# Kernel tuning notes

Measured on AMD Instinct MI355X. Metric: run time of the kernel, lower is better.

Reference implementation:

```python
import jax, jax.numpy as jnp
import numpy as np

THRESHOLD = 0.1
N_HEAD = 16
NEG_INF = -1e9


def setup_inputs() -> dict:
    key = jax.random.key(0)
    ks = jax.random.split(key, 8)
    B, T, C = 2, 2048, 1024
    H, D, R = N_HEAD, C // N_HEAD, 8
    return {
        "x": jax.random.normal(ks[0], (B, T, C), dtype=jnp.float32),
        "W_attn": jax.random.normal(ks[1], (C, 3 * C), dtype=jnp.float32) * 0.02,
        "W_proj": jax.random.normal(ks[2], (C, C), dtype=jnp.float32) * 0.02,
        "W_recip": jax.random.normal(ks[3], (D, R), dtype=jnp.float32) * 0.02,
        "w_std": jax.random.uniform(ks[4], (H,), dtype=jnp.float32),
        "w_rec": jax.random.uniform(ks[5], (H,), dtype=jnp.float32),
        "w_disc": jax.random.uniform(ks[6], (H,), dtype=jnp.float32),
        "d_bias": jax.random.normal(ks[7], (H, T), dtype=jnp.float32) * 0.02,
    }


def reference(x, W_attn, W_proj, W_recip, w_std, w_rec, w_disc, d_bias):
    B, T, C = x.shape
    H = N_HEAD
    D = C // H
    R = W_recip.shape[1]
    D_std = D - R

    # QKV projection (Linear without bias)
    qkv = x @ W_attn  # [B,T,3C]
    q, k, v = jnp.split(qkv, 3, axis=2)

    def to_heads(t):
        return t.reshape(B, T, H, D).transpose(0, 2, 1, 3)  # [B,H,T,D]

    q, k, v = to_heads(q), to_heads(k), to_heads(v)

    # low-rank reciprocal projections
    QW = q @ W_recip  # [B,H,T,R]
    KW = k @ W_recip

    ws = jnp.sqrt(jnp.clip(w_std, 1e-8))[:, None, None]  # [H,1,1]
    wr = jnp.sqrt(jnp.clip(w_rec, 1e-8))[:, None, None]
    use_ra = (w_rec > THRESHOLD)[:, None, None]  # [H,1,1]

    # RA heads: augmented Q/K = [ws*Q_std | wr*KW] / [ws*K_std | wr*QW]
    q_aug = jnp.concatenate([ws * q[..., :D_std], wr * KW], axis=-1)
    k_aug = jnp.concatenate([ws * k[..., :D_std], wr * QW], axis=-1)
    q_eff = jnp.where(use_ra, q_aug, ws * q)
    k_eff = jnp.where(use_ra, k_aug, ws * k)

    # mean-centered discoverability column bias: [1,H,1,T]
    d = d_bias[:, :T]
    d = d - d.mean(axis=-1, keepdims=True)
    bias = (d * w_disc[:, None])[None, :, None, :]

    scale = 1.0 / jnp.sqrt(jnp.asarray(D, dtype=x.dtype))
    scores = jnp.einsum("bhid,bhjd->bhij", q_eff, k_eff) * scale + bias
    causal = jnp.tril(jnp.ones((T, T), dtype=bool))
    scores = jnp.where(causal[None, None], scores, NEG_INF)
    attn = jax.nn.softmax(scores, axis=-1)
    out = jnp.einsum("bhij,bhjd->bhid", attn, v)  # [B,H,T,D]

    out = out.transpose(0, 2, 1, 3).reshape(B, T, C)
    return out @ W_proj
```

## Files before the change

### kernel.cpp

```cpp
#include <hip/hip_runtime.h>
#include <hip/hip_bf16.h>

#define DEVI __device__ __forceinline__

typedef __attribute__((ext_vector_type(8))) short short8;
typedef __attribute__((ext_vector_type(4))) short short4v;
typedef __attribute__((ext_vector_type(4))) float floatx4;

static constexpr int B_ = 2, T_ = 2048, C_ = 1024, H_ = 16, D_ = 64;
static constexpr float LOG2E = 1.44269504088896f;

DEVI float bf2f(unsigned short u) {
    union { unsigned int i; float f; } v; v.i = ((unsigned int)u) << 16; return v.f;
}
DEVI unsigned short f2bf(float f) {
    union { float f; unsigned int i; } v; v.f = f;
    unsigned int x = v.i;
    return (unsigned short)((x + 0x7fffu + ((x >> 16) & 1u)) >> 16);
}
DEVI unsigned int pk2bf(float lo, float hi) {
#if __has_builtin(__builtin_amdgcn_cvt_pk_bf16_f32)
    typedef __attribute__((ext_vector_type(2))) __bf16 bf16x2;
    union { bf16x2 v; unsigned int u; } r;
    r.v = __builtin_amdgcn_cvt_pk_bf16_f32(lo, hi);
    return r.u;
#else
    return (unsigned int)f2bf(lo) | ((unsigned int)f2bf(hi) << 16);
#endif
}
DEVI float fast_exp2(float x) {
#if __has_builtin(__builtin_amdgcn_exp2f)
    return __builtin_amdgcn_exp2f(x);
#else
    return __expf(x * 0.6931471805599453f);
#endif
}

DEVI void async16(const unsigned short* g, unsigned short* l) {
    __builtin_amdgcn_global_load_lds((const __attribute__((address_space(1))) void*)g,
                                     (__attribute__((address_space(3))) void*)l, 16, 0, 0);
}

DEVI void tr_body(const float* in, unsigned short* out, int K, int N, int bx, int by,
                  int tid, float (*tile)[65]) {
    int k0 = by * 64, n0 = bx * 64;
#pragma unroll
    for (int r = 0; r < 4; r++) {
        int ci = tid + r * 256;
        int row = ci >> 4, c4 = (ci & 15) * 4;
        float4 v = *(const float4*)&in[(size_t)(k0 + row) * N + n0 + c4];
        tile[row][c4 + 0] = v.x; tile[row][c4 + 1] = v.y;
        tile[row][c4 + 2] = v.z; tile[row][c4 + 3] = v.w;
    }
    __syncthreads();
#pragma unroll
    for (int r = 0; r < 2; r++) {
        int ci = tid + r * 256;
        int row = ci >> 3, c8 = (ci & 7) * 8;
        union { unsigned short u[8]; short8 s; } o;
#pragma unroll
        for (int j = 0; j < 8; j++) o.u[j] = f2bf(tile[c8 + j][row]);
        *(short8*)&out[(size_t)(n0 + row) * K + k0 + c8] = o.s;
    }
}

__global__ __launch_bounds__(256) void k_prep(const float* __restrict__ x,
                                              const float* __restrict__ W_attn,
                                              const float* __restrict__ W_proj,
                                              const float* __restrict__ d_bias,
                                              const float* __restrict__ w_disc,
                                              unsigned short* __restrict__ x_bf,
                                              unsigned short* __restrict__ wa_t,
                                              unsigned short* __restrict__ wp_t,
                                              float* __restrict__ bias) {
    __shared__ float tile[64][65];
    __shared__ float red[256];
    int bid = blockIdx.x, tid = threadIdx.x;
    if (bid < 2048) {
        int i = bid * 256 + tid;
        const float4* p = (const float4*)x + (size_t)i * 2;
        float4 a = p[0], b = p[1];
        union { unsigned short u[8]; short8 s; } r;
        r.u[0] = f2bf(a.x); r.u[1] = f2bf(a.y); r.u[2] = f2bf(a.z); r.u[3] = f2bf(a.w);
        r.u[4] = f2bf(b.x); r.u[5] = f2bf(b.y); r.u[6] = f2bf(b.z); r.u[7] = f2bf(b.w);
        *(short8*)&x_bf[(size_t)i * 8] = r.s;
    } else if (bid < 2816) {
        int idx = bid - 2048;
        tr_body(W_attn, wa_t, 1024, 3072, idx % 48, idx / 48, tid, tile);
    } else if (bid < 3072) {
        int idx = bid - 2816;
        tr_body(W_proj, wp_t, 1024, 1024, idx & 15, idx >> 4, tid, tile);
    } else {
        int h = bid - 3072;
        float s = 0.f;
        for (int t = tid; t < T_; t += 256) s += d_bias[h * T_ + t];
        red[tid] = s;
        __syncthreads();
        for (int st = 128; st > 0; st >>= 1) {
            if (tid < st) red[tid] += red[tid + st];
            __syncthreads();
        }
        float mean = red[0] * (1.0f / T_);
        float wd = w_disc[h] * LOG2E;
        for (int t = tid; t < T_; t += 256) bias[h * T_ + t] = (d_bias[h * T_ + t] - mean) * wd;
    }
}

template <typename OUT>
__global__ __launch_bounds__(256) void k_gemm(const unsigned short* __restrict__ A,
                                              const unsigned short* __restrict__ Bt,
                                              OUT* __restrict__ C, int M, int N, int K) {
    __shared__ __align__(16) unsigned short As[128 * 32];
    __shared__ __align__(16) unsigned short Bs[128 * 32];
    int m0 = blockIdx.y * 128, n0 = blockIdx.x * 128;
    int tid = threadIdx.x, l = tid & 63, w = tid >> 6;
    int wm = (w >> 1) * 64, wn = (w & 1) * 64;
    int lm = l & 15, lq = l >> 4;
    floatx4 acc[4][4];
#pragma unroll
    for (int a = 0; a < 4; a++)
#pragma unroll
        for (int b = 0; b < 4; b++) acc[a][b] = {0.f, 0.f, 0.f, 0.f};

    for (int k0 = 0; k0 < K; k0 += 32) {
        __syncthreads();
#pragma unroll
        for (int r = 0; r < 2; r++) {
            int ci = tid + r * 256;
            int row = ci >> 2, off = (ci & 3) * 8;
            async16(&A[(size_t)(m0 + row) * K + k0 + off], &As[row * 32 + off]);
            async16(&Bt[(size_t)(n0 + row) * K + k0 + off], &Bs[row * 32 + off]);
        }
        __syncthreads();
        short8 af[4], bf[4];
#pragma unroll
        for (int t = 0; t < 4; t++) af[t] = *(short8*)&As[(wm + t * 16 + lm) * 32 + lq * 8];
#pragma unroll
        for (int t = 0; t < 4; t++) bf[t] = *(short8*)&Bs[(wn + t * 16 + lm) * 32 + lq * 8];
#pragma unroll
        for (int tm = 0; tm < 4; tm++)
#pragma unroll
            for (int tn = 0; tn < 4; tn++)
                acc[tm][tn] = __builtin_amdgcn_mfma_f32_16x16x32_bf16(af[tm], bf[tn], acc[tm][tn], 0, 0, 0);
    }
#pragma unroll
    for (int tm = 0; tm < 4; tm++)
#pragma unroll
        for (int tn = 0; tn < 4; tn++) {
            int row = m0 + wm + tm * 16 + lq * 4;
            int col = n0 + wn + tn * 16 + lm;
#pragma unroll
            for (int r = 0; r < 4; r++) {
                float v = acc[tm][tn][r];
                if constexpr (sizeof(OUT) == 2) C[(size_t)(row + r) * N + col] = (OUT)f2bf(v);
                else                            C[(size_t)(row + r) * N + col] = v;
            }
        }
}

__global__ __launch_bounds__(256) void k_gemm64(const unsigned short* __restrict__ A,
                                                const unsigned short* __restrict__ Bt,
                                                float* __restrict__ C, int M, int N, int K) {
    __shared__ __align__(16) unsigned short As[128 * 32];
    __shared__ __align__(16) unsigned short Bs[64 * 32];
    int m0 = blockIdx.y * 128, n0 = blockIdx.x * 64;
    int tid = threadIdx.x, l = tid & 63, w = tid >> 6;
    int wm = w * 32;
    int lm = l & 15, lq = l >> 4;
    floatx4 acc[2][4];
#pragma unroll
    for (int a = 0; a < 2; a++)
#pragma unroll
        for (int b = 0; b < 4; b++) acc[a][b] = {0.f, 0.f, 0.f, 0.f};

    for (int k0 = 0; k0 < K; k0 += 32) {
        __syncthreads();
#pragma unroll
        for (int r = 0; r < 2; r++) {
            int ci = tid + r * 256;
            int row = ci >> 2, off = (ci & 3) * 8;
            async16(&A[(size_t)(m0 + row) * K + k0 + off], &As[row * 32 + off]);
        }
        {
            int row = tid >> 2, off = (tid & 3) * 8;
            async16(&Bt[(size_t)(n0 + row) * K + k0 + off], &Bs[row * 32 + off]);
        }
        __syncthreads();
        short8 af[2], bf[4];
#pragma unroll
        for (int t = 0; t < 2; t++) af[t] = *(short8*)&As[(wm + t * 16 + lm) * 32 + lq * 8];
#pragma unroll
        for (int t = 0; t < 4; t++) bf[t] = *(short8*)&Bs[(t * 16 + lm) * 32 + lq * 8];
#pragma unroll
        for (int tm = 0; tm < 2; tm++)
#pragma unroll
            for (int tn = 0; tn < 4; tn++)
                acc[tm][tn] = __builtin_amdgcn_mfma_f32_16x16x32_bf16(af[tm], bf[tn], acc[tm][tn], 0, 0, 0);
    }
#pragma unroll
    for (int tm = 0; tm < 2; tm++)
#pragma unroll
        for (int tn = 0; tn < 4; tn++) {
            int row = m0 + wm + tm * 16 + lq * 4;
            int col = n0 + tn * 16 + lm;
#pragma unroll
            for (int r = 0; r < 4; r++) C[(size_t)(row + r) * N + col] = acc[tm][tn][r];
        }
}

DEVI void build_body(const unsigned short* qkv, const float* Wr, const float* w_std,
                     const float* w_rec, unsigned short* qe, unsigned short* ke, int g) {
    int t = g & (T_ - 1), h = (g >> 11) & (H_ - 1), b = g >> 15;
    float ws = sqrtf(fmaxf(w_std[h], 1e-8f));
    float wr = sqrtf(fmaxf(w_rec[h], 1e-8f));
    bool ra = w_rec[h] > 0.1f;
    const unsigned short* qrow = qkv + (size_t)(b * T_ + t) * 3072 + h * 64;
    const unsigned short* krow = qrow + 1024;
    float q[64], k[64];
#pragma unroll
    for (int i = 0; i < 8; i++) {
        short8 qv = *(const short8*)&qrow[i * 8];
        short8 kv = *(const short8*)&krow[i * 8];
#pragma unroll
        for (int j = 0; j < 8; j++) {
            q[i * 8 + j] = bf2f((unsigned short)qv[j]);
            k[i * 8 + j] = bf2f((unsigned short)kv[j]);
        }
    }
    float QW[8], KW[8];
#pragma unroll
    for (int r = 0; r < 8; r++) { QW[r] = 0.f; KW[r] = 0.f; }
#pragma unroll
    for (int d = 0; d < 64; d++)
#pragma unroll
        for (int r = 0; r < 8; r++) {
            QW[r] += q[d] * Wr[d * 8 + r];
            KW[r] += k[d] * Wr[d * 8 + r];
        }
    const float qscale = 0.125f * LOG2E;
    size_t tbase = (size_t)(b * H_ + h) * 131072 + (size_t)(t >> 4) * 1024 + (size_t)(t & 15) * 8;
#pragma unroll
    for (int i = 0; i < 8; i++) {
        union { unsigned short u[8]; short8 s; } uq, uk;
#pragma unroll
        for (int j = 0; j < 8; j++) {
            int d = i * 8 + j;
            float qv, kv;
            if (ra && d >= 56) { qv = wr * KW[d - 56]; kv = wr * QW[d - 56]; }
            else               { qv = ws * q[d];       kv = ws * k[d]; }
            uq.u[j] = f2bf(qv * qscale);
            uk.u[j] = f2bf(kv);
        }
        size_t off = tbase + (size_t)(i >> 2) * 512 + (size_t)(i & 3) * 128;
        *(short8*)&qe[off] = uq.s;
        *(short8*)&ke[off] = uk.s;
    }
}

__global__ __launch_bounds__(256) void k_bv(const unsigned short* __restrict__ qkv,
                                            const float* __restrict__ W_recip,
                                            const float* __restrict__ w_std,
                                            const float* __restrict__ w_rec,
                                            unsigned short* __restrict__ qe,
                                            unsigned short* __restrict__ ke,
                                            unsigned short* __restrict__ vt) {
    __shared__ float Wr[64 * 8];
    int bid = blockIdx.x, tid = threadIdx.x;
    if (bid < 256) {
        for (int i = tid; i < 512; i += 256) Wr[i] = W_recip[i];
        __syncthreads();
        build_body(qkv, Wr, w_std, w_rec, qe, ke, bid * 256 + tid);
    } else {
        int g = bid - 256;
        int tchunk = g & 63;
        int h = (g >> 6) & 15, b = g >> 10;
        int d = tid & 63, tg = tid >> 6;
        int t0 = tchunk * 32 + tg * 8;
        union { unsigned short u[8]; short8 s; } v;
#pragma unroll
        for (int i = 0; i < 8; i++)
            v.u[i] = qkv[(size_t)(b * T_ + t0 + i) * 3072 + 2048 + h * 64 + d];
        size_t off = (size_t)((b * H_ + h)) * 131072 + (size_t)tchunk * 2048 +
                     (size_t)(d >> 4) * 512 + (size_t)tg * 128 + (size_t)(d & 15) * 8;
        *(short8*)&vt[off] = v.s;
    }
}

DEVI void exp_pack(float sv[4][4], float& l_part, unsigned int pk[4][2]) {
#pragma unroll
    for (int js = 0; js < 4; js++)
#pragma unroll
        for (int r = 0; r < 4; r++) {
            float p = fast_exp2(sv[js][r]);
            sv[js][r] = p;
            l_part += p;
        }
#pragma unroll
    for (int js = 0; js < 4; js++) {
        pk[js][0] = pk2bf(sv[js][0], sv[js][1]);
        pk[js][1] = pk2bf(sv[js][2], sv[js][3]);
    }
}

DEVI short8 make_pf(const unsigned int pk[4][2], int c, int srcLo, int srcHi, bool hi) {
    int a0 = __shfl((int)pk[2 * c][0], srcLo);
    int a1 = __shfl((int)pk[2 * c][1], srcLo);
    int a2 = __shfl((int)pk[2 * c][0], srcHi);
    int a3 = __shfl((int)pk[2 * c][1], srcHi);
    int b0 = __shfl((int)pk[2 * c + 1][0], srcLo);
    int b1 = __shfl((int)pk[2 * c + 1][1], srcLo);
    int b2 = __shfl((int)pk[2 * c + 1][0], srcHi);
    int b3 = __shfl((int)pk[2 * c + 1][1], srcHi);
    union { int i[4]; short8 s; } pf;
    pf.i[0] = hi ? b0 : a0;
    pf.i[1] = hi ? b1 : a1;
    pf.i[2] = hi ? b2 : a2;
    pf.i[3] = hi ? b3 : a3;
    return pf.s;
}

struct KF { short8 lo[4]; short8 hi[4]; };

__global__ __launch_bounds__(256) void k_attn(const unsigned short* __restrict__ qe,
                                              const unsigned short* __restrict__ ke,
                                              const unsigned short* __restrict__ vt,
                                              const float* __restrict__ bias,
                                              unsigned short* __restrict__ obf) {
    int bh = blockIdx.y;
    int b = bh >> 4, h = bh & 15;
    int tid = threadIdx.x, l = tid & 63, w = tid >> 6;
    int lm = l & 15, lq = l >> 4;
    int l8 = l * 8;
    const size_t hb = (size_t)bh * 131072;
    const unsigned short* qeh = qe + hb;
    const unsigned short* keh = ke + hb;
    const unsigned short* vth = vt + hb;
    const float* biash = bias + h * T_;

    int gA = blockIdx.x * 4 + w;
    int gB = 127 - gA;
    int itA = (gA >> 2) + 1, itB = (gB >> 2) + 1;
    int irowA = gA * 16 + lm, irowB = gB * 16 + lm;

    short8 qA0 = *(const short8*)(qeh + (size_t)gA * 1024 + l8);
    short8 qA1 = *(const short8*)(qeh + (size_t)gA * 1024 + 512 + l8);
    short8 qB0 = *(const short8*)(qeh + (size_t)gB * 1024 + l8);
    short8 qB1 = *(const short8*)(qeh + (size_t)gB * 1024 + 512 + l8);

    floatx4 OA[4], OB[4];
#pragma unroll
    for (int i = 0; i < 4; i++) { OA[i] = {0.f, 0.f, 0.f, 0.f}; OB[i] = {0.f, 0.f, 0.f, 0.f}; }
    float lA = 0.f, lB = 0.f;

    const int srcLo = ((lq & 1) * 2) * 16 + lm;
    const int srcHi = srcLo + 16;
    const bool hi = (lq >> 1) & 1;

    KF kfa, kfb;
#pragma unroll
    for (int js = 0; js < 4; js++) {
        const unsigned short* kp = keh + (size_t)js * 1024 + l8;
        kfa.lo[js] = *(const short8*)kp;
        kfa.hi[js] = *(const short8*)(kp + 512);
    }

    auto step = [&](int s, KF& cur, KF& nxt) {
        int j0 = s * 64;
        bool doA = (s < itA);
        bool maskA = (s == itA - 1);
        bool maskB = (s == itB - 1);
        {
            const unsigned short* kb = keh + (size_t)(s + 1) * 4096 + l8;
#pragma unroll
            for (int js = 0; js < 4; js++) {
                nxt.lo[js] = *(const short8*)(kb + js * 1024);
                nxt.hi[js] = *(const short8*)(kb + js * 1024 + 512);
            }
        }
        short8 vfr[2][4];
#pragma unroll
        for (int c = 0; c < 2; c++)
#pragma unroll
            for (int dt = 0; dt < 4; dt++)
                vfr[c][dt] = *(const short8*)(vth + (size_t)((j0 >> 5) + c) * 2048 + dt * 512 + l8);
        float bv[4][4];
#pragma unroll
        for (int js = 0; js < 4; js++) {
            float4 bj = *(const float4*)&biash[j0 + js * 16 + lq * 4];
            bv[js][0] = bj.x; bv[js][1] = bj.y; bv[js][2] = bj.z; bv[js][3] = bj.w;
        }
        floatx4 sb4[4], sa4[4];
#pragma unroll
        for (int js = 0; js < 4; js++) {
            floatx4 sb = {0.f, 0.f, 0.f, 0.f};
            sb = __builtin_amdgcn_mfma_f32_16x16x32_bf16(cur.lo[js], qB0, sb, 0, 0, 0);
            sb = __builtin_amdgcn_mfma_f32_16x16x32_bf16(cur.hi[js], qB1, sb, 0, 0, 0);
            sb4[js] = sb;
        }
        if (doA) {
#pragma unroll
            for (int js = 0; js < 4; js++) {
                floatx4 sa = {0.f, 0.f, 0.f, 0.f};
                sa = __builtin_amdgcn_mfma_f32_16x16x32_bf16(cur.lo[js], qA0, sa, 0, 0, 0);
                sa = __builtin_amdgcn_mfma_f32_16x16x32_bf16(cur.hi[js], qA1, sa, 0, 0, 0);
                sa4[js] = sa;
            }
        }
        float svB[4][4];
#pragma unroll
        for (int js = 0; js < 4; js++)
#pragma unroll
            for (int r = 0; r < 4; r++) svB[js][r] = sb4[js][r] + bv[js][r];
        if (maskB) {
#pragma unroll
            for (int js = 0; js < 4; js++) {
                int jb = j0 + js * 16 + lq * 4;
#pragma unroll
                for (int r = 0; r < 4; r++)
                    if (jb + r > irowB) svB[js][r] = -1e9f;
            }
        }
        unsigned int pkB[4][2];
        exp_pack(svB, lB, pkB);

        if (doA) {
            float svA[4][4];
#pragma unroll
            for (int js = 0; js < 4; js++)
#pragma unroll
                for (int r = 0; r < 4; r++) svA[js][r] = sa4[js][r] + bv[js][r];
            if (maskA) {
#pragma unroll
                for (int js = 0; js < 4; js++) {
                    int jb = j0 + js * 16 + lq * 4;
#pragma unroll
                    for (int r = 0; r < 4; r++)
                        if (jb + r > irowA) svA[js][r] = -1e9f;
                }
            }
            unsigned int pkA[4][2];
            exp_pack(svA, lA, pkA);
#pragma unroll
            for (int c = 0; c < 2; c++) {
                short8 pfA = make_pf(pkA, c, srcLo, srcHi, hi);
                short8 pfB = make_pf(pkB, c, srcLo, srcHi, hi);
#pragma unroll
                for (int dt = 0; dt < 4; dt++) {
                    OA[dt] = __builtin_amdgcn_mfma_f32_16x16x32_bf16(vfr[c][dt], pfA, OA[dt], 0, 0, 0);
                    OB[dt] = __builtin_amdgcn_mfma_f32_16x16x32_bf16(vfr[c][dt], pfB, OB[dt], 0, 0, 0);
                }
            }
        } else {
#pragma unroll
            for (int c = 0; c < 2; c++) {
                short8 pfB = make_pf(pkB, c, srcLo, srcHi, hi);
#pragma unroll
                for (int dt = 0; dt < 4; dt++)
                    OB[dt] = __builtin_amdgcn_mfma_f32_16x16x32_bf16(vfr[c][dt], pfB, OB[dt], 0, 0, 0);
            }
        }
    };

    int s = 0;
    for (; s + 2 <= itB; s += 2) {
        step(s, kfa, kfb);
        step(s + 1, kfb, kfa);
    }
    if (s < itB) step(s, kfa, kfb);

    lA += __shfl_xor(lA, 16); lA += __shfl_xor(lA, 32);
    lB += __shfl_xor(lB, 16); lB += __shfl_xor(lB, 32);
    {
        float inv = 1.0f / lA;
        unsigned short* orow = obf + (size_t)(b * T_ + irowA) * C_ + h * 64;
#pragma unroll
        for (int dt = 0; dt < 4; dt++) {
            union { unsigned short u[4]; short4v s4; } o;
#pragma unroll
            for (int r = 0; r < 4; r++) o.u[r] = f2bf(OA[dt][r] * inv);
            *(short4v*)&orow[dt * 16 + lq * 4] = o.s4;
        }
    }
    {
        float inv = 1.0f / lB;
        unsigned short* orow = obf + (size_t)(b * T_ + irowB) * C_ + h * 64;
#pragma unroll
        for (int dt = 0; dt < 4; dt++) {
            union { unsigned short u[4]; short4v s4; } o;
#pragma unroll
            for (int r = 0; r < 4; r++) o.u[r] = f2bf(OB[dt][r] * inv);
            *(short4v*)&orow[dt * 16 + lq * 4] = o.s4;
        }
    }
}

extern "C" void kernel_launch(void* const* d_in, const int* in_sizes, int n_in,
                              void* d_out, int out_size, void* d_ws, size_t ws_size,
                              hipStream_t stream) {
    const float* x       = (const float*)d_in[0];
    const float* W_attn  = (const float*)d_in[1];
    const float* W_proj  = (const float*)d_in[2];
    const float* W_recip = (const float*)d_in[3];
    const float* w_std   = (const float*)d_in[4];
    const float* w_rec   = (const float*)d_in[5];
    const float* w_disc  = (const float*)d_in[6];
    const float* d_bias  = (const float*)d_in[7];

    char* ws = (char*)d_ws;
    size_t o = 0;
    unsigned short* x_bf = (unsigned short*)(ws + o); o += (size_t)4096 * 1024 * 2;
    unsigned short* wa_t = (unsigned short*)(ws + o); o += (size_t)3072 * 1024 * 2;
    unsigned short* wp_t = (unsigned short*)(ws + o); o += (size_t)1024 * 1024 * 2;
    unsigned short* qkv  = (unsigned short*)(ws + o); o += (size_t)4096 * 3072 * 2;
    unsigned short* qe   = (unsigned short*)(ws + o); o += (size_t)32 * 2048 * 64 * 2;
    unsigned short* ke   = (unsigned short*)(ws + o); o += (size_t)32 * 2048 * 64 * 2;
    unsigned short* vt   = (unsigned short*)(ws + o); o += (size_t)32 * 2048 * 64 * 2;
    unsigned short* obf  = (unsigned short*)(ws + o); o += (size_t)4096 * 1024 * 2;
    float* bias          = (float*)(ws + o);          o += (size_t)16 * 2048 * 4;

    k_prep<<<3088, 256, 0, stream>>>(x, W_attn, W_proj, d_bias, w_disc, x_bf, wa_t, wp_t, bias);
    k_gemm<unsigned short><<<dim3(24, 32), 256, 0, stream>>>(x_bf, wa_t, qkv, 4096, 3072, 1024);
    k_bv<<<2304, 256, 0, stream>>>(qkv, W_recip, w_std, w_rec, qe, ke, vt);
    k_attn<<<dim3(16, 32), 256, 0, stream>>>(qe, ke, vt, bias, obf);
    k_gemm64<<<dim3(16, 32), 256, 0, stream>>>(obf, wp_t, (float*)d_out, 4096, 1024, 1024);
}
```

Baseline: 206.9 us.

## Fuse QKV head-building epilogue into QKV GEMM and prefetch attention bias

The QKV GEMM weights are permuted so each 128-column tile holds one head's Q and K (or two heads' V). The GEMM epilogue then computes the low-rank reciprocal projections and writes qe/ke/vt in the attention layout directly. This removes the bf16 qkv intermediate buffer and the separate k_bv kernel. The attention loop also prefetches the next tile's bias alongside K, at the cost of more registers and a larger LDS footprint in the GEMM.

```diff
diff --git a/kernel.cpp b/kernel.cpp
--- a/kernel.cpp
+++ b/kernel.cpp
@@ -41,9 +41,8 @@
                                      (__attribute__((address_space(3))) void*)l, 16, 0, 0);
 }
 
-DEVI void tr_body(const float* in, unsigned short* out, int K, int N, int bx, int by,
+DEVI void tr_body(const float* in, unsigned short* out_base, int K, int N, int n0, int k0,
                   int tid, float (*tile)[65]) {
-    int k0 = by * 64, n0 = bx * 64;
 #pragma unroll
     for (int r = 0; r < 4; r++) {
         int ci = tid + r * 256;
@@ -60,7 +59,7 @@
         union { unsigned short u[8]; short8 s; } o;
 #pragma unroll
         for (int j = 0; j < 8; j++) o.u[j] = f2bf(tile[c8 + j][row]);
-        *(short8*)&out[(size_t)(n0 + row) * K + k0 + c8] = o.s;
+        *(short8*)&out_base[(size_t)row * K + k0 + c8] = o.s;
     }
 }
 
@@ -86,10 +85,16 @@
         *(short8*)&x_bf[(size_t)i * 8] = r.s;
     } else if (bid < 2816) {
         int idx = bid - 2048;
-        tr_body(W_attn, wa_t, 1024, 3072, idx % 48, idx / 48, tid, tile);
+        int n0 = (idx % 48) * 64, k0 = (idx / 48) * 64;
+        int p0;
+        if (n0 < 1024)      p0 = (n0 >> 6) * 128;
+        else if (n0 < 2048) p0 = ((n0 - 1024) >> 6) * 128 + 64;
+        else                p0 = n0;
+        tr_body(W_attn, wa_t + (size_t)p0 * 1024, 1024, 3072, n0, k0, tid, tile);
     } else if (bid < 3072) {
         int idx = bid - 2816;
-        tr_body(W_proj, wp_t, 1024, 1024, idx & 15, idx >> 4, tid, tile);
+        int n0 = (idx & 15) * 64, k0 = (idx >> 4) * 64;
+        tr_body(W_proj, wp_t + (size_t)n0 * 1024, 1024, 1024, n0, k0, tid, tile);
     } else {
         int h = bid - 3072;
         float s = 0.f;
@@ -106,16 +111,24 @@
     }
 }
 
-template <typename OUT>
-__global__ __launch_bounds__(256) void k_gemm(const unsigned short* __restrict__ A,
-                                              const unsigned short* __restrict__ Bt,
-                                              OUT* __restrict__ C, int M, int N, int K) {
-    __shared__ __align__(16) unsigned short As[128 * 32];
-    __shared__ __align__(16) unsigned short Bs[128 * 32];
-    int m0 = blockIdx.y * 128, n0 = blockIdx.x * 128;
+__global__ __launch_bounds__(256) void k_gemm_qkv(const unsigned short* __restrict__ A,
+                                                  const unsigned short* __restrict__ Bt,
+                                                  const float* __restrict__ W_recip,
+                                                  const float* __restrict__ w_std,
+                                                  const float* __restrict__ w_rec,
+                                                  unsigned short* __restrict__ qe,
+                                                  unsigned short* __restrict__ ke,
+                                                  unsigned short* __restrict__ vt) {
+    __shared__ __align__(16) char smem[45056];
+    unsigned short* As = (unsigned short*)smem;
+    unsigned short* Bs = (unsigned short*)(smem + 8192);
+    float* Wr = (float*)(smem + 34816);
+    const int K = 1024;
+    int m0 = blockIdx.y * 128, bx = blockIdx.x, n0 = bx * 128;
     int tid = threadIdx.x, l = tid & 63, w = tid >> 6;
     int wm = (w >> 1) * 64, wn = (w & 1) * 64;
     int lm = l & 15, lq = l >> 4;
+    for (int i = tid; i < 512; i += 256) Wr[i] = W_recip[i];
     floatx4 acc[4][4];
 #pragma unroll
     for (int a = 0; a < 4; a++)
@@ -143,19 +156,77 @@
             for (int tn = 0; tn < 4; tn++)
                 acc[tm][tn] = __builtin_amdgcn_mfma_f32_16x16x32_bf16(af[tm], bf[tn], acc[tm][tn], 0, 0, 0);
     }
-#pragma unroll
-    for (int tm = 0; tm < 4; tm++)
-#pragma unroll
-        for (int tn = 0; tn < 4; tn++) {
-            int row = m0 + wm + tm * 16 + lq * 4;
-            int col = n0 + wn + tn * 16 + lm;
-#pragma unroll
-            for (int r = 0; r < 4; r++) {
-                float v = acc[tm][tn][r];
-                if constexpr (sizeof(OUT) == 2) C[(size_t)(row + r) * N + col] = (OUT)f2bf(v);
-                else                            C[(size_t)(row + r) * N + col] = v;
-            }
-        }
+    __syncthreads();
+
+    if (bx < 16) {
+        int h = bx;
+        unsigned short* epi = (unsigned short*)smem;
+#pragma unroll
+        for (int tm = 0; tm < 4; tm++)
+#pragma unroll
+            for (int tn = 0; tn < 4; tn++)
+#pragma unroll
+                for (int r = 0; r < 4; r++)
+                    epi[(wm + tm * 16 + lq * 4 + r) * 136 + wn + tn * 16 + lm] =
+                        f2bf(acc[tm][tn][r]);
+        __syncthreads();
+        float* ldsw = (float*)(smem + 36864);
+        int row = tid >> 1, side = tid & 1;
+        float v64[64];
+        const unsigned short* rp = epi + row * 136 + side * 64;
+#pragma unroll
+        for (int i = 0; i < 8; i++) {
+            short8 s8 = *(const short8*)&rp[i * 8];
+#pragma unroll
+            for (int j = 0; j < 8; j++) v64[i * 8 + j] = bf2f((unsigned short)s8[j]);
+        }
+        float W8[8];
+#pragma unroll
+        for (int r = 0; r < 8; r++) W8[r] = 0.f;
+#pragma unroll
+        for (int d = 0; d < 64; d++)
+#pragma unroll
+            for (int r = 0; r < 8; r++) W8[r] += v64[d] * Wr[d * 8 + r];
+#pragma unroll
+        for (int r = 0; r < 8; r++) ldsw[row * 16 + side * 8 + r] = W8[r];
+        __syncthreads();
+        float ws_ = sqrtf(fmaxf(w_std[h], 1e-8f));
+        float wr_ = sqrtf(fmaxf(w_rec[h], 1e-8f));
+        bool ra = w_rec[h] > 0.1f;
+        const float* other = &ldsw[row * 16 + (side ^ 1) * 8];
+        int m = m0 + row, b = m >> 11, t = m & 2047;
+        size_t tbase = (size_t)(b * 16 + h) * 131072 + (size_t)(t >> 4) * 1024 + (size_t)(t & 15) * 8;
+        float scale = side ? 1.0f : 0.125f * LOG2E;
+        unsigned short* outp = side ? ke : qe;
+#pragma unroll
+        for (int i = 0; i < 8; i++) {
+            union { unsigned short u[8]; short8 s; } o;
+#pragma unroll
+            for (int j = 0; j < 8; j++) {
+                int d = i * 8 + j;
+                float val = (ra && d >= 56) ? wr_ * other[d - 56] : ws_ * v64[d];
+                o.u[j] = f2bf(val * scale);
+            }
+            *(short8*)&outp[tbase + (size_t)(i >> 2) * 512 + (size_t)(i & 3) * 128] = o.s;
+        }
+    } else {
+        int j2 = bx - 16;
+        int h = 2 * j2 + (w & 1);
+#pragma unroll
+        for (int tm = 0; tm < 4; tm++) {
+            int t0g = m0 + wm + tm * 16 + lq * 4;
+            int bb = t0g >> 11, tl = t0g & 2047;
+            size_t base = (size_t)(bb * 16 + h) * 131072 + (size_t)(tl >> 5) * 2048 +
+                          (size_t)((tl >> 3) & 3) * 128 + (size_t)(tl & 7);
+#pragma unroll
+            for (int tn = 0; tn < 4; tn++) {
+                union { unsigned short u[4]; short4v s; } o;
+#pragma unroll
+                for (int r = 0; r < 4; r++) o.u[r] = f2bf(acc[tm][tn][r]);
+                *(short4v*)&vt[base + (size_t)tn * 512 + (size_t)lm * 8] = o.s;
+            }
+        }
+    }
 }
 
 __global__ __launch_bounds__(256) void k_gemm64(const unsigned short* __restrict__ A,
@@ -206,84 +277,6 @@
 #pragma unroll
             for (int r = 0; r < 4; r++) C[(size_t)(row + r) * N + col] = acc[tm][tn][r];
         }
-}
-
-DEVI void build_body(const unsigned short* qkv, const float* Wr, const float* w_std,
-                     const float* w_rec, unsigned short* qe, unsigned short* ke, int g) {
-    int t = g & (T_ - 1), h = (g >> 11) & (H_ - 1), b = g >> 15;
-    float ws = sqrtf(fmaxf(w_std[h], 1e-8f));
-    float wr = sqrtf(fmaxf(w_rec[h], 1e-8f));
-    bool ra = w_rec[h] > 0.1f;
-    const unsigned short* qrow = qkv + (size_t)(b * T_ + t) * 3072 + h * 64;
-    const unsigned short* krow = qrow + 1024;
-    float q[64], k[64];
-#pragma unroll
-    for (int i = 0; i < 8; i++) {
-        short8 qv = *(const short8*)&qrow[i * 8];
-        short8 kv = *(const short8*)&krow[i * 8];
-#pragma unroll
-        for (int j = 0; j < 8; j++) {
-            q[i * 8 + j] = bf2f((unsigned short)qv[j]);
-            k[i * 8 + j] = bf2f((unsigned short)kv[j]);
-        }
-    }
-    float QW[8], KW[8];
-#pragma unroll
-    for (int r = 0; r < 8; r++) { QW[r] = 0.f; KW[r] = 0.f; }
-#pragma unroll
-    for (int d = 0; d < 64; d++)
-#pragma unroll
-        for (int r = 0; r < 8; r++) {
-            QW[r] += q[d] * Wr[d * 8 + r];
-            KW[r] += k[d] * Wr[d * 8 + r];
-        }
-    const float qscale = 0.125f * LOG2E;
-    size_t tbase = (size_t)(b * H_ + h) * 131072 + (size_t)(t >> 4) * 1024 + (size_t)(t & 15) * 8;
-#pragma unroll
-    for (int i = 0; i < 8; i++) {
-        union { unsigned short u[8]; short8 s; } uq, uk;
-#pragma unroll
-        for (int j = 0; j < 8; j++) {
-            int d = i * 8 + j;
-            float qv, kv;
-            if (ra && d >= 56) { qv = wr * KW[d - 56]; kv = wr * QW[d - 56]; }
-            else               { qv = ws * q[d];       kv = ws * k[d]; }
-            uq.u[j] = f2bf(qv * qscale);
-            uk.u[j] = f2bf(kv);
-        }
-        size_t off = tbase + (size_t)(i >> 2) * 512 + (size_t)(i & 3) * 128;
-        *(short8*)&qe[off] = uq.s;
-        *(short8*)&ke[off] = uk.s;
-    }
-}
-
-__global__ __launch_bounds__(256) void k_bv(const unsigned short* __restrict__ qkv,
-                                            const float* __restrict__ W_recip,
-                                            const float* __restrict__ w_std,
-                                            const float* __restrict__ w_rec,
-                                            unsigned short* __restrict__ qe,
-                                            unsigned short* __restrict__ ke,
-                                            unsigned short* __restrict__ vt) {
-    __shared__ float Wr[64 * 8];
-    int bid = blockIdx.x, tid = threadIdx.x;
-    if (bid < 256) {
-        for (int i = tid; i < 512; i += 256) Wr[i] = W_recip[i];
-        __syncthreads();
-        build_body(qkv, Wr, w_std, w_rec, qe, ke, bid * 256 + tid);
-    } else {
-        int g = bid - 256;
-        int tchunk = g & 63;
-        int h = (g >> 6) & 15, b = g >> 10;
-        int d = tid & 63, tg = tid >> 6;
-        int t0 = tchunk * 32 + tg * 8;
-        union { unsigned short u[8]; short8 s; } v;
-#pragma unroll
-        for (int i = 0; i < 8; i++)
-            v.u[i] = qkv[(size_t)(b * T_ + t0 + i) * 3072 + 2048 + h * 64 + d];
-        size_t off = (size_t)((b * H_ + h)) * 131072 + (size_t)tchunk * 2048 +
-                     (size_t)(d >> 4) * 512 + (size_t)tg * 128 + (size_t)(d & 15) * 8;
-        *(short8*)&vt[off] = v.s;
-    }
 }
 
 DEVI void exp_pack(float sv[4][4], float& l_part, unsigned int pk[4][2]) {
@@ -320,6 +313,7 @@
 }
 
 struct KF { short8 lo[4]; short8 hi[4]; };
+struct BV { float4 q[4]; };
 
 __global__ __launch_bounds__(256) void k_attn(const unsigned short* __restrict__ qe,
                                               const unsigned short* __restrict__ ke,
@@ -357,24 +351,28 @@
     const bool hi = (lq >> 1) & 1;
 
     KF kfa, kfb;
+    BV bva, bvb;
 #pragma unroll
     for (int js = 0; js < 4; js++) {
         const unsigned short* kp = keh + (size_t)js * 1024 + l8;
         kfa.lo[js] = *(const short8*)kp;
         kfa.hi[js] = *(const short8*)(kp + 512);
-    }
-
-    auto step = [&](int s, KF& cur, KF& nxt) {
+        bva.q[js] = *(const float4*)&biash[js * 16 + lq * 4];
+    }
+
+    auto step = [&](int s, KF& cur, KF& nxt, BV& bcur, BV& bnxt) {
         int j0 = s * 64;
         bool doA = (s < itA);
         bool maskA = (s == itA - 1);
         bool maskB = (s == itB - 1);
+        int sp = (s + 1 < itB) ? s + 1 : s;
         {
             const unsigned short* kb = keh + (size_t)(s + 1) * 4096 + l8;
 #pragma unroll
             for (int js = 0; js < 4; js++) {
                 nxt.lo[js] = *(const short8*)(kb + js * 1024);
                 nxt.hi[js] = *(const short8*)(kb + js * 1024 + 512);
+                bnxt.q[js] = *(const float4*)&biash[sp * 64 + js * 16 + lq * 4];
             }
         }
         short8 vfr[2][4];
@@ -383,12 +381,6 @@
 #pragma unroll
             for (int dt = 0; dt < 4; dt++)
                 vfr[c][dt] = *(const short8*)(vth + (size_t)((j0 >> 5) + c) * 2048 + dt * 512 + l8);
-        float bv[4][4];
-#pragma unroll
-        for (int js = 0; js < 4; js++) {
-            float4 bj = *(const float4*)&biash[j0 + js * 16 + lq * 4];
-            bv[js][0] = bj.x; bv[js][1] = bj.y; bv[js][2] = bj.z; bv[js][3] = bj.w;
-        }
         floatx4 sb4[4], sa4[4];
 #pragma unroll
         for (int js = 0; js < 4; js++) {
@@ -408,9 +400,12 @@
         }
         float svB[4][4];
 #pragma unroll
-        for (int js = 0; js < 4; js++)
-#pragma unroll
-            for (int r = 0; r < 4; r++) svB[js][r] = sb4[js][r] + bv[js][r];
+        for (int js = 0; js < 4; js++) {
+            svB[js][0] = sb4[js][0] + bcur.q[js].x;
+            svB[js][1] = sb4[js][1] + bcur.q[js].y;
+            svB[js][2] = sb4[js][2] + bcur.q[js].z;
+            svB[js][3] = sb4[js][3] + bcur.q[js].w;
+        }
         if (maskB) {
 #pragma unroll
             for (int js = 0; js < 4; js++) {
@@ -426,9 +421,12 @@
         if (doA) {
             float svA[4][4];
 #pragma unroll
-            for (int js = 0; js < 4; js++)
-#pragma unroll
-                for (int r = 0; r < 4; r++) svA[js][r] = sa4[js][r] + bv[js][r];
+            for (int js = 0; js < 4; js++) {
+                svA[js][0] = sa4[js][0] + bcur.q[js].x;
+                svA[js][1] = sa4[js][1] + bcur.q[js].y;
+                svA[js][2] = sa4[js][2] + bcur.q[js].z;
+                svA[js][3] = sa4[js][3] + bcur.q[js].w;
+            }
             if (maskA) {
 #pragma unroll
                 for (int js = 0; js < 4; js++) {
@@ -463,10 +461,10 @@
 
     int s = 0;
     for (; s + 2 <= itB; s += 2) {
-        step(s, kfa, kfb);
-        step(s + 1, kfb, kfa);
-    }
-    if (s < itB) step(s, kfa, kfb);
+        step(s, kfa, kfb, bva, bvb);
+        step(s + 1, kfb, kfa, bvb, bva);
+    }
+    if (s < itB) step(s, kfa, kfb, bva, bvb);
 
     lA += __shfl_xor(lA, 16); lA += __shfl_xor(lA, 32);
     lB += __shfl_xor(lB, 16); lB += __shfl_xor(lB, 32);
@@ -511,7 +509,6 @@
     unsigned short* x_bf = (unsigned short*)(ws + o); o += (size_t)4096 * 1024 * 2;
     unsigned short* wa_t = (unsigned short*)(ws + o); o += (size_t)3072 * 1024 * 2;
     unsigned short* wp_t = (unsigned short*)(ws + o); o += (size_t)1024 * 1024 * 2;
-    unsigned short* qkv  = (unsigned short*)(ws + o); o += (size_t)4096 * 3072 * 2;
     unsigned short* qe   = (unsigned short*)(ws + o); o += (size_t)32 * 2048 * 64 * 2;
     unsigned short* ke   = (unsigned short*)(ws + o); o += (size_t)32 * 2048 * 64 * 2;
     unsigned short* vt   = (unsigned short*)(ws + o); o += (size_t)32 * 2048 * 64 * 2;
@@ -519,8 +516,7 @@
     float* bias          = (float*)(ws + o);          o += (size_t)16 * 2048 * 4;
 
     k_prep<<<3088, 256, 0, stream>>>(x, W_attn, W_proj, d_bias, w_disc, x_bf, wa_t, wp_t, bias);
-    k_gemm<unsigned short><<<dim3(24, 32), 256, 0, stream>>>(x_bf, wa_t, qkv, 4096, 3072, 1024);
-    k_bv<<<2304, 256, 0, stream>>>(qkv, W_recip, w_std, w_rec, qe, ke, vt);
+    k_gemm_qkv<<<dim3(24, 32), 256, 0, stream>>>(x_bf, wa_t, W_recip, w_std, w_rec, qe, ke, vt);
     k_attn<<<dim3(16, 32), 256, 0, stream>>>(qe, ke, vt, bias, obf);
     k_gemm64<<<dim3(16, 32), 256, 0, stream>>>(obf, wp_t, (float*)d_out, 4096, 1024, 1024);
 }
```

Result: slower. 226.2 us (+9.3%).
